# Optimization experiments

Measured on AMD Instinct MI355X. Metric: run time of the kernel, lower is better.

The kernel has to match this reference:

```python
import jax, jax.numpy as jnp
import numpy as np

EPS = 1e-5
GROUPS = 4


def _bn(x, g, b, axes):
    # training-mode batch norm (fresh torch module runs in train mode): biased var
    mean = x.mean(axes, keepdims=True)
    var = x.var(axes, keepdims=True)
    sh = (1, -1) + (1,) * (x.ndim - 2)
    return (x - mean) * jax.lax.rsqrt(var + EPS) * g.reshape(sh) + b.reshape(sh)


def _prelu(x, a):
    return jnp.where(x >= 0, x, a * x)


def _avgpool2(x):
    B, C, H, W = x.shape
    return x.reshape(B, C, H // 2, 2, W // 2, 2).mean(axis=(3, 5))


def _axial(x, dim, qkv_w, qkv_g, qkv_b, sim_g, sim_b, rel_emb, out_g, out_b):
    # x: [B, C, H, W]; dim==0 attends over H, dim==1 over W
    if dim == 0:
        x = jnp.transpose(x, (0, 3, 1, 2))  # [B, W, C, H]
    else:
        x = jnp.transpose(x, (0, 2, 1, 3))  # [B, H, C, W]
    B, D1, C, A = x.shape
    x = x.reshape(B * D1, C, A)
    # 1x1 conv1d (no bias) + BN1d
    qkv = jnp.einsum('oc,nca->noa', qkv_w, x)
    qkv = _bn(qkv, qkv_g, qkv_b, axes=(0, 2))
    gc = qkv.shape[1] // GROUPS // 2  # group_channels
    qkv = qkv.reshape(B * D1, GROUPS, 2 * gc, A)
    q = qkv[:, :, : gc // 2]
    k = qkv[:, :, gc // 2: gc]
    v = qkv[:, :, gc:]
    # relative position embeddings gathered into [2*gc, A, A]
    ri = jnp.arange(A)[:, None] - jnp.arange(A)[None, :] + A - 1  # [A, A]
    emb = rel_emb[:, ri]
    qe, ke, ve = emb[: gc // 2], emb[gc // 2: gc], emb[gc:]
    q_emb = jnp.einsum('ngci,cij->ngij', q, qe)
    k_emb = jnp.einsum('ngci,cij->ngij', k, ke)
    qk = jnp.einsum('ngci,ngcj->ngij', q_emb, k_emb)
    sim = jnp.concatenate([qk, q_emb, k_emb], axis=1)  # [N, 3g, A, A]
    sim = _bn(sim, sim_g, sim_b, axes=(0, 2, 3))
    sim = sim.reshape(B * D1, 3, GROUPS, A, A).sum(axis=1)
    sim = jax.nn.softmax(sim, axis=3)
    am = jnp.einsum('ngij,ngcj->ngci', sim, v)
    ame = jnp.einsum('ngij,cij->ngci', sim, ve)
    # cat along last dim then view -> equivalent to stacking pairs on a new axis
    out = jnp.stack([am, ame], axis=3).reshape(B * D1, 2 * GROUPS * gc, A)
    out = _bn(out, out_g, out_b, axes=(0, 2))
    out = out.reshape(B, D1, GROUPS * gc, 2, A).sum(axis=3)
    if dim == 0:
        return jnp.transpose(out, (0, 2, 3, 1))  # [B, C_out, H, W]
    return jnp.transpose(out, (0, 2, 1, 3))


def _cbn(x, g, b, lin_w, latent):
    x = _bn(x, g, b, axes=(0, 2, 3))
    sb = lin_w @ latent  # [2*C]
    C = x.shape[1]
    scale, bias = sb[:C], sb[C:]
    return scale[None, :, None, None] * x + bias[None, :, None, None]


def _forward(input, latent_vector, w_in, cbn1_g, cbn1_b, cbn1_lin, prelu1,
             ax0_qkv_w, ax0_qkv_g, ax0_qkv_b, ax0_sim_g, ax0_sim_b, ax0_rel_emb, ax0_out_g, ax0_out_b,
             ax1_qkv_w, ax1_qkv_g, ax1_qkv_b, ax1_sim_g, ax1_sim_b, ax1_rel_emb, ax1_out_g, ax1_out_b,
             w_out, cbn2_g, cbn2_b, cbn2_lin, prelu2):
    out = jnp.einsum('oc,bchw->bohw', w_in, input)
    out = _prelu(_cbn(out, cbn1_g, cbn1_b, cbn1_lin, latent_vector), prelu1)
    out = _axial(out, 0, ax0_qkv_w, ax0_qkv_g, ax0_qkv_b, ax0_sim_g, ax0_sim_b, ax0_rel_emb, ax0_out_g, ax0_out_b)
    out = _axial(out, 1, ax1_qkv_w, ax1_qkv_g, ax1_qkv_b, ax1_sim_g, ax1_sim_b, ax1_rel_emb, ax1_out_g, ax1_out_b)
    out = _avgpool2(out)
    out = jnp.einsum('oc,bchw->bohw', w_out, out)
    out = _cbn(out, cbn2_g, cbn2_b, cbn2_lin, latent_vector)
    out = out + _avgpool2(input)  # residual_mapping is Identity (in==out channels)
    return _prelu(out, prelu2)


def setup_inputs() -> dict:
    key = jax.random.key(0)
    ks = jax.random.split(key, 12)
    C, L, S = 64, 256, 128
    gc = C // GROUPS  # 16
    d = {}
    d['input'] = jax.random.normal(ks[0], (4, C, S, S), dtype=jnp.float32)
    d['latent_vector'] = jax.random.normal(ks[1], (L,), dtype=jnp.float32)
    d['w_in'] = jax.random.normal(ks[2], (C, C), dtype=jnp.float32) * 0.1
    d['cbn1_g'] = jnp.ones((C,), jnp.float32)
    d['cbn1_b'] = jnp.zeros((C,), jnp.float32)
    d['cbn1_lin'] = jax.random.normal(ks[3], (2 * C, L), dtype=jnp.float32) * 0.05
    d['prelu1'] = jnp.float32(0.25)
    for i, k1, k2 in [(0, ks[4], ks[5]), (1, ks[6], ks[7])]:
        d[f'ax{i}_qkv_w'] = jax.random.normal(k1, (2 * C, C), dtype=jnp.float32) * 0.1
        d[f'ax{i}_qkv_g'] = jnp.ones((2 * C,), jnp.float32)
        d[f'ax{i}_qkv_b'] = jnp.zeros((2 * C,), jnp.float32)
        d[f'ax{i}_sim_g'] = jnp.ones((3 * GROUPS,), jnp.float32)
        d[f'ax{i}_sim_b'] = jnp.zeros((3 * GROUPS,), jnp.float32)
        d[f'ax{i}_rel_emb'] = jax.random.normal(k2, (2 * gc, 2 * S - 1), dtype=jnp.float32)
        d[f'ax{i}_out_g'] = jnp.ones((2 * C,), jnp.float32)
        d[f'ax{i}_out_b'] = jnp.zeros((2 * C,), jnp.float32)
    d['w_out'] = jax.random.normal(ks[8], (C, C), dtype=jnp.float32) * 0.1
    d['cbn2_g'] = jnp.ones((C,), jnp.float32)
    d['cbn2_b'] = jnp.zeros((C,), jnp.float32)
    d['cbn2_lin'] = jax.random.normal(ks[9], (2 * C, L), dtype=jnp.float32) * 0.05
    d['prelu2'] = jnp.float32(0.25)
    return d


def reference(input, latent_vector, w_in, cbn1_g, cbn1_b, cbn1_lin, prelu1,
              ax0_qkv_w, ax0_qkv_g, ax0_qkv_b, ax0_sim_g, ax0_sim_b, ax0_rel_emb, ax0_out_g, ax0_out_b,
              ax1_qkv_w, ax1_qkv_g, ax1_qkv_b, ax1_sim_g, ax1_sim_b, ax1_rel_emb, ax1_out_g, ax1_out_b,
              w_out, cbn2_g, cbn2_b, cbn2_lin, prelu2):
    return _forward(input, latent_vector, w_in, cbn1_g, cbn1_b, cbn1_lin, prelu1,
                    ax0_qkv_w, ax0_qkv_g, ax0_qkv_b, ax0_sim_g, ax0_sim_b, ax0_rel_emb, ax0_out_g, ax0_out_b,
                    ax1_qkv_w, ax1_qkv_g, ax1_qkv_b, ax1_sim_g, ax1_sim_b, ax1_rel_emb, ax1_out_g, ax1_out_b,
                    w_out, cbn2_g, cbn2_b, cbn2_lin, prelu2)
```

## Files before the change

kernel.cpp:

```cpp
#include <hip/hip_runtime.h>

#define EPS 1e-5f
#define SP 16

typedef __attribute__((ext_vector_type(4))) _Float16 h4;
typedef __attribute__((ext_vector_type(8))) _Float16 h8;
typedef __attribute__((ext_vector_type(4))) float f4;
typedef __attribute__((ext_vector_type(4))) unsigned int u4;

#define WS_SB1        0
#define WS_SB2        128
#define WS_STAT_C1    256
#define WS_STAT_QKV0  2304
#define WS_STAT_QKV1  6400
#define WS_STAT_SIM0  10496
#define WS_STAT_SIM1  10880
#define WS_STAT_OUT0  11264
#define WS_STAT_OUT1  15360
#define WS_STAT_C2    19456
#define WS_STAT_END   21504

#define WS_R1  32768
#define WS_R2  (WS_R1 + 8388608)
#define WS_R3  (WS_R2 + 8388608)

#define SIM_CNT_INV (1.f / 2097152.f)

#define L_QEA 0
#define L_KEB 32768
#define L_RET 65536
#define L_AQ  73728
#define L_AK  77824
#define L_V   73728

__device__ __forceinline__ float wred(float v) {
    #pragma unroll
    for (int off = 32; off > 0; off >>= 1) v += __shfl_down(v, off, 64);
    return v;
}

__global__ void k_prep0(const float* __restrict__ lin1, const float* __restrict__ lin2,
                        const float* __restrict__ latent, float* __restrict__ ws) {
    int t = threadIdx.x;
    for (int i = 256 + t; i < WS_STAT_END; i += 256) ws[i] = 0.f;
    const float* lin = (t < 128) ? lin1 : lin2;
    int row = t & 127;
    float s = 0.f;
    for (int l = 0; l < 256; ++l) s += lin[row * 256 + l] * latent[l];
    ws[(t < 128 ? WS_SB1 : WS_SB2) + row] = s;
}

__global__ __launch_bounds__(256) void k_conv1(const float* __restrict__ in,
                                               const float* __restrict__ w,
                                               float* __restrict__ out) {
    __shared__ float ws_[4096];
    int t = threadIdx.x;
    for (int i = t; i < 4096; i += 256) ws_[i] = w[i];
    __syncthreads();
    int p  = blockIdx.x * 256 + t;
    int b  = p >> 14, hw = p & 16383;
    const float* ip = in + b * 64 * 16384 + hw;
    float x[64];
    #pragma unroll
    for (int c = 0; c < 64; ++c) x[c] = ip[c * 16384];
    float* op = out + b * 64 * 16384 + hw;
    for (int o = 0; o < 64; ++o) {
        float acc = 0.f;
        #pragma unroll
        for (int c = 0; c < 64; ++c) acc += ws_[o * 64 + c] * x[c];
        op[o * 16384] = acc;
    }
}

__global__ void k_stats(const float* __restrict__ src, int C, int logK, int MK, int split,
                        float* __restrict__ stat) {
    int c = blockIdx.x % C;
    int chunk = blockIdx.x / C;
    int per = MK / split;
    int base = chunk * per;
    int Km1 = (1 << logK) - 1;
    float s = 0.f, ss = 0.f;
    for (int i = base + threadIdx.x; i < base + per; i += blockDim.x) {
        int m = i >> logK, k = i & Km1;
        float v = src[((m * C + c) << logK) + k];
        s += v; ss += v * v;
    }
    s = wred(s); ss = wred(ss);
    if ((threadIdx.x & 63) == 0) { atomicAdd(&stat[c * SP], s); atomicAdd(&stat[(C + c) * SP], ss); }
}

__global__ __launch_bounds__(256) void k_t1t(const float* __restrict__ src, float* __restrict__ dst,
                                             const float* __restrict__ ws,
                                             const float* __restrict__ g1,
                                             const float* __restrict__ b1,
                                             const float* __restrict__ prelu1) {
    __shared__ float tile[32][33];
    int bid = blockIdx.x;
    int wt = bid & 3, ht = (bid >> 2) & 3, c = (bid >> 4) & 63, b = bid >> 10;
    float mean = ws[WS_STAT_C1 + c * SP] * (1.f / 65536.f);
    float var  = ws[WS_STAT_C1 + (64 + c) * SP] * (1.f / 65536.f) - mean * mean;
    float ab = g1[c] * rsqrtf(var + EPS);
    float sc = ws[WS_SB1 + c], bi = ws[WS_SB1 + 64 + c];
    float A = sc * ab;
    float Bb = sc * (b1[c] - mean * ab) + bi;
    float slope = *prelu1;
    int tx = threadIdx.x & 31, ty = threadIdx.x >> 5;
    const float* sp = src + ((b * 64 + c) * 128 + ht * 32) * 128 + wt * 32;
    for (int r = 0; r < 4; ++r) {
        float v = sp[(ty + r * 8) * 128 + tx];
        v = A * v + Bb;
        v = v >= 0.f ? v : slope * v;
        tile[ty + r * 8][tx] = v;
    }
    __syncthreads();
    float* dp = dst + b * 1048576 + (wt * 32) * 8192 + c * 128 + ht * 32;
    for (int r = 0; r < 4; ++r)
        dp[(ty + r * 8) * 8192 + tx] = tile[tx][ty + r * 8];
}

__global__ __launch_bounds__(256) void k_qkvm(const float* __restrict__ x, const float* __restrict__ w,
                                              _Float16* __restrict__ out, float* __restrict__ statq,
                                              int SB, int SR, int SC) {
    __shared__ __align__(16) _Float16 Wh[8192];
    __shared__ __align__(16) _Float16 Xt[8192];
    int t = threadIdx.x;
    int lane = t & 63, wv = t >> 6;
    int l15 = lane & 15, g4 = lane >> 4;
    int n = (blockIdx.x & 7) * 64 + (blockIdx.x >> 3);
    int b = n >> 7, r = n & 127;
    for (int i = t; i < 8192; i += 256) {
        int o = i >> 6, c = i & 63;
        Wh[o * 64 + (c ^ ((o & 7) << 3))] = (_Float16)w[i];
    }
    const float* xp = x + b * SB + r * SR;
    for (int i = t; i < 8192; i += 256) {
        int c = i >> 7, a = i & 127;
        Xt[a * 64 + (c ^ ((a & 7) << 3))] = (_Float16)xp[c * SC + a];
    }
    __syncthreads();
    _Float16* op = out + n * 16384;
    float sA[2][4] = {{0.f,0.f,0.f,0.f},{0.f,0.f,0.f,0.f}};
    float qA[2][4] = {{0.f,0.f,0.f,0.f},{0.f,0.f,0.f,0.f}};
    #pragma unroll
    for (int ot2 = 0; ot2 < 2; ++ot2) {
        int orow = (wv * 2 + ot2) * 16 + l15;
        h8 af[2];
        #pragma unroll
        for (int kk = 0; kk < 2; ++kk)
            af[kk] = *(const h8*)&Wh[orow * 64 + ((kk * 32 + g4 * 8) ^ ((orow & 7) << 3))];
        #pragma unroll
        for (int at = 0; at < 8; ++at) {
            int arow = at * 16 + l15;
            f4 c4 = {0.f, 0.f, 0.f, 0.f};
            #pragma unroll
            for (int kk = 0; kk < 2; ++kk) {
                h8 bf = *(const h8*)&Xt[arow * 64 + ((kk * 32 + g4 * 8) ^ ((arow & 7) << 3))];
                c4 = __builtin_amdgcn_mfma_f32_16x16x32_f16(af[kk], bf, c4, 0, 0, 0);
            }
            #pragma unroll
            for (int r4 = 0; r4 < 4; ++r4) {
                int o = (wv * 2 + ot2) * 16 + g4 * 4 + r4;
                float v = c4[r4];
                op[o * 128 + at * 16 + l15] = (_Float16)v;
                sA[ot2][r4] += v; qA[ot2][r4] += v * v;
            }
        }
    }
    #pragma unroll
    for (int ot2 = 0; ot2 < 2; ++ot2)
        #pragma unroll
        for (int r4 = 0; r4 < 4; ++r4) {
            float s = sA[ot2][r4], ss = qA[ot2][r4];
            #pragma unroll
            for (int msk = 1; msk < 16; msk <<= 1) {
                s += __shfl_xor(s, msk, 64); ss += __shfl_xor(ss, msk, 64);
            }
            if (l15 == 0) {
                int o = (wv * 2 + ot2) * 16 + g4 * 4 + r4;
                atomicAdd(&statq[o * SP], s);
                atomicAdd(&statq[(128 + o) * SP], ss);
            }
        }
}

__device__ __forceinline__ void stage_aqk(unsigned char* L, const _Float16* qkv,
                                          const float* statq, const float* qg, const float* qb,
                                          int n, int g, int t) {
    const _Float16* qp = qkv + n * 16384 + g * 32 * 128;
    #pragma unroll
    for (int k = 0; k < 4; ++k) {
        int i = t + k * 512;
        int a = i & 127, cc = i >> 7;
        int ch = g * 32 + cc;
        float mean = statq[ch * SP] * (1.f / 65536.f);
        float var  = statq[(128 + ch) * SP] * (1.f / 65536.f) - mean * mean;
        float A = qg[ch] * rsqrtf(var + EPS);
        float B = qb[ch] - mean * A;
        float v = A * (float)qp[cc * 128 + a] + B;
        _Float16 h = (_Float16)v;
        int off = a * 32 + ((cc * 2) ^ ((a & 4) << 2));
        *(_Float16*)(L + L_AQ + off) = (cc < 8) ? h : (_Float16)0.f;
        *(_Float16*)(L + L_AK + off) = (cc < 8) ? (_Float16)0.f : h;
    }
}

__device__ __forceinline__ void stage_ret(unsigned char* L, const float* remb, int crow0, int t) {
    #pragma unroll
    for (int k = 0; k < 8; ++k) {
        int i = t + k * 512;
        int d = i & 255, c = i >> 8;
        float v = (d < 255) ? remb[(crow0 + c) * 255 + d] : 0.f;
        *(_Float16*)(L + L_RET + d * 32 + ((c * 2) ^ ((d & 4) << 2))) = (_Float16)v;
    }
}

template <bool STATS>
__device__ __forceinline__ void build_emb(unsigned char* L, int w, int l15, int g4, float* s) {
    int at = w;
    int arow = at * 16 + l15;
    int aoff = arow * 32 + ((g4 * 8) ^ ((arow & 4) << 2));
    h4 aq = *(const h4*)(L + L_AQ + aoff);
    h4 ak = *(const h4*)(L + L_AK + aoff);
    int abase = at * 16 + g4 * 4;
    #pragma unroll
    for (int m = 0; m < 9; ++m) {
        int drow = (at + m) * 16 + l15;
        h4 bf = *(const h4*)(L + L_RET + drow * 32 + ((g4 * 8) ^ ((drow & 4) << 2)));
        f4 z = {0.f, 0.f, 0.f, 0.f};
        f4 dq = __builtin_amdgcn_mfma_f32_16x16x16f16(aq, bf, z, 0, 0, 0);
        f4 dk = __builtin_amdgcn_mfma_f32_16x16x16f16(ak, bf, z, 0, 0, 0);
        #pragma unroll
        for (int r = 0; r < 4; ++r) {
            int a = abase + r;
            int b = 127 + a - drow;
            bool ok = (m == 0 || m == 8) ? (b >= 0 && b < 128) : true;
            if (ok) {
                int off = b * 256 + ((a * 2) ^ ((b & 7) << 4));
                *(_Float16*)(L + L_QEA + off) = (_Float16)dq[r];
                *(_Float16*)(L + L_KEB + off) = (_Float16)dk[r];
                if (STATS) {
                    s[0] += dq[r]; s[1] += dq[r] * dq[r];
                    s[2] += dk[r]; s[3] += dk[r] * dk[r];
                }
            }
        }
    }
}

__device__ __forceinline__ void qk_mfma(unsigned char* L, int i0, int l15, int g4, f4 acc[8]) {
    h8 af[4];
    #pragma unroll
    for (int ks = 0; ks < 4; ++ks) {
        int row = i0 + l15;
        af[ks] = *(const h8*)(L + L_QEA + row * 256 + ((ks * 64 + g4 * 16) ^ ((row & 7) << 4)));
    }
    #pragma unroll
    for (int tj = 0; tj < 8; ++tj) {
        h8 bf[4];
        #pragma unroll
        for (int ks = 0; ks < 4; ++ks) {
            int row = tj * 16 + l15;
            bf[ks] = *(const h8*)(L + L_KEB + row * 256 + ((ks * 64 + g4 * 16) ^ ((row & 7) << 4)));
        }
        f4 c = {0.f, 0.f, 0.f, 0.f};
        #pragma unroll
        for (int ks = 0; ks < 4; ++ks)
            c = __builtin_amdgcn_mfma_f32_16x16x32_f16(af[ks], bf[ks], c, 0, 0, 0);
        acc[tj] = c;
    }
}

__global__ __launch_bounds__(512, 4) void k_passA(const _Float16* __restrict__ qkv,
                                                  const float* __restrict__ remb,
                                                  const float* __restrict__ statq,
                                                  const float* __restrict__ qg,
                                                  const float* __restrict__ qb,
                                                  float* __restrict__ statsim) {
    __shared__ __align__(16) unsigned char L[81920];
    int t = threadIdx.x;
    int lane = t & 63, w = t >> 6;
    int l15 = lane & 15, g4 = lane >> 4;
    int ts = (blockIdx.x & 7) * 64 + (blockIdx.x >> 3);
    int n = (ts >> 2) * 4, g = ts & 3;

    stage_aqk(L, qkv, statq, qg, qb, n, g, t);
    stage_ret(L, remb, 0, t);
    __syncthreads();

    float es[4] = {0.f, 0.f, 0.f, 0.f};
    build_emb<true>(L, w, l15, g4, es);
    __syncthreads();

    float* red = (float*)(L + L_AK);
    #pragma unroll
    for (int k = 0; k < 4; ++k) es[k] = wred(es[k]);
    if (lane == 0) {
        red[w * 4 + 0] = es[0]; red[w * 4 + 1] = es[1];
        red[w * 4 + 2] = es[2]; red[w * 4 + 3] = es[3];
    }

    f4 acc[8];
    qk_mfma(L, w * 16, l15, g4, acc);

    float s = 0.f, ss = 0.f;
    #pragma unroll
    for (int tj = 0; tj < 8; ++tj)
        #pragma unroll
        for (int r = 0; r < 4; ++r) { float x = acc[tj][r]; s += x; ss += x * x; }
    s = wred(s); ss = wred(ss);
    if (lane == 0) { red[32 + w * 2] = s; red[33 + w * 2] = ss; }
    __syncthreads();

    if (t < 6) {
        float v = 0.f;
        int dst;
        if (t == 0)      { for (int k = 0; k < 8; ++k) v += red[32 + 2 * k]; dst = g; }
        else if (t == 1) { for (int k = 0; k < 8; ++k) v += red[33 + 2 * k]; dst = 12 + g; }
        else if (t == 2) { for (int k = 0; k < 8; ++k) v += red[k * 4 + 0];  dst = 4 + g; }
        else if (t == 3) { for (int k = 0; k < 8; ++k) v += red[k * 4 + 1];  dst = 16 + g; }
        else if (t == 4) { for (int k = 0; k < 8; ++k) v += red[k * 4 + 2];  dst = 8 + g; }
        else             { for (int k = 0; k < 8; ++k) v += red[k * 4 + 3];  dst = 20 + g; }
        atomicAdd(&statsim[dst * SP], v);
    }
}

__global__ __launch_bounds__(512, 4) void k_passB(const _Float16* __restrict__ qkv,
                                                  const float* __restrict__ remb,
                                                  const float* __restrict__ statq,
                                                  const float* __restrict__ qg,
                                                  const float* __restrict__ qb,
                                                  const float* __restrict__ statsim,
                                                  const float* __restrict__ simg,
                                                  const float* __restrict__ simb,
                                                  unsigned int* __restrict__ att2,
                                                  float* __restrict__ statout) {
    __shared__ __align__(16) unsigned char L[81920];
    int t = threadIdx.x;
    int lane = t & 63, w = t >> 6;
    int l15 = lane & 15, g4 = lane >> 4;
    int s0 = (blockIdx.x & 7) * 256 + (blockIdx.x >> 3);
    int n = s0 >> 2, g = s0 & 3;

    stage_aqk(L, qkv, statq, qg, qb, n, g, t);
    stage_ret(L, remb, 0, t);
    __syncthreads();

    build_emb<false>(L, w, l15, g4, nullptr);
    __syncthreads();

    #pragma unroll
    for (int k = 0; k < 4; ++k) {
        int i = t + k * 512;
        int j = i & 127, c = i >> 7;
        int ch = g * 32 + 16 + c;
        float mean = statq[ch * SP] * (1.f / 65536.f);
        float var  = statq[(128 + ch) * SP] * (1.f / 65536.f) - mean * mean;
        float A = qg[ch] * rsqrtf(var + EPS);
        float B = qb[ch] - mean * A;
        float v = A * (float)qkv[n * 16384 + ch * 128 + j] + B;
        *(_Float16*)(L + L_V + c * 256 + ((j * 2) ^ ((c & 7) << 4))) = (_Float16)v;
    }
    #pragma unroll
    for (int k = 0; k < 8; ++k) {
        int i = t + k * 512;
        int d = i & 255, c = i >> 8;
        float v = (d < 255) ? remb[(16 + c) * 255 + d] : 0.f;
        *(_Float16*)(L + L_RET + c * 512 + ((d * 2) ^ ((c & 7) << 4))) = (_Float16)v;
    }

    int i0 = w * 16;
    f4 acc[8];
    qk_mfma(L, i0, l15, g4, acc);

    float Aqk, Aqe, Ake, Cst = 0.f;
    {
        float A3[3];
        #pragma unroll
        for (int k = 0; k < 3; ++k) {
            int ch = k * 4 + g;
            float mean = statsim[ch * SP] * SIM_CNT_INV;
            float var  = statsim[(12 + ch) * SP] * SIM_CNT_INV - mean * mean;
            float A = simg[ch] * rsqrtf(var + EPS);
            A3[k] = A;
            Cst += simb[ch] - mean * A;
        }
        Aqk = A3[0]; Aqe = A3[1]; Ake = A3[2];
    }
    int ib = (i0 + g4 * 4) * 2;
    #pragma unroll
    for (int tj = 0; tj < 8; ++tj) {
        int j = tj * 16 + l15;
        h4 q4 = *(const h4*)(L + L_QEA + j * 256 + (ib ^ ((j & 7) << 4)));
        h4 k4 = *(const h4*)(L + L_KEB + j * 256 + (ib ^ ((j & 7) << 4)));
        #pragma unroll
        for (int r = 0; r < 4; ++r)
            acc[tj][r] = Aqk * acc[tj][r] + Aqe * (float)q4[r] + Ake * (float)k4[r] + Cst;
    }

    float inv4[4];
    #pragma unroll
    for (int r = 0; r < 4; ++r) {
        float m = acc[0][r];
        #pragma unroll
        for (int tj = 1; tj < 8; ++tj) m = fmaxf(m, acc[tj][r]);
        #pragma unroll
        for (int msk = 1; msk < 16; msk <<= 1) m = fmaxf(m, __shfl_xor(m, msk, 64));
        float s = 0.f;
        #pragma unroll
        for (int tj = 0; tj < 8; ++tj) {
            float e = __expf(acc[tj][r] - m);
            acc[tj][r] = e; s += e;
        }
        #pragma unroll
        for (int msk = 1; msk < 16; msk <<= 1) s += __shfl_xor(s, msk, 64);
        inv4[r] = 1.f / s;
    }

    _Float16 ph[4][8];
    #pragma unroll
    for (int r = 0; r < 4; ++r)
        #pragma unroll
        for (int tj = 0; tj < 8; ++tj)
            ph[r][tj] = (_Float16)(acc[tj][r] * inv4[r]);
    __syncthreads();

    #pragma unroll
    for (int r = 0; r < 4; ++r) {
        int i = i0 + g4 * 4 + r;
        int swz = (i & 7) << 4;
        #pragma unroll
        for (int tj = 0; tj < 8; ++tj) {
            int j = tj * 16 + l15;
            _Float16 h = ph[r][tj];
            *(_Float16*)(L + L_QEA + i * 256 + ((j * 2) ^ swz)) = h;
            int cl = (j >= i) ? (127 + i - j) : j;
            *(_Float16*)(L + L_KEB + i * 256 + ((cl * 2) ^ swz)) = (j >= i) ? h : (_Float16)0.f;
        }
    }
    __syncthreads();

    h8 vf[4], vef[4];
    #pragma unroll
    for (int ks = 0; ks < 4; ++ks) {
        vf[ks]  = *(const h8*)(L + L_V   + l15 * 256 + ((ks * 64 + g4 * 16) ^ ((l15 & 7) << 4)));
        vef[ks] = *(const h8*)(L + L_RET + l15 * 512 + ((ks * 64 + g4 * 16) ^ ((l15 & 7) << 4)));
    }
    int row = i0 + l15;
    int sw = (row & 7) << 4;
    f4 cam = {0.f, 0.f, 0.f, 0.f}, cae = {0.f, 0.f, 0.f, 0.f};
    #pragma unroll
    for (int ks = 0; ks < 4; ++ks) {
        h8 pf  = *(const h8*)(L + L_QEA + row * 256 + ((ks * 64 + g4 * 16) ^ sw));
        h8 plf = *(const h8*)(L + L_KEB + row * 256 + ((ks * 64 + g4 * 16) ^ sw));
        cam = __builtin_amdgcn_mfma_f32_16x16x32_f16(vf[ks],  pf,  cam, 0, 0, 0);
        cae = __builtin_amdgcn_mfma_f32_16x16x32_f16(vef[ks], plf, cae, 0, 0, 0);
    }
    __syncthreads();

    #pragma unroll
    for (int r = 0; r < 4; ++r) {
        int i = i0 + g4 * 4 + r;
        int swz = (i & 7) << 4;
        #pragma unroll
        for (int tj = 0; tj < 8; ++tj) {
            int j = tj * 16 + l15;
            int cl = (j < i) ? (i - 1 - j) : j;
            *(_Float16*)(L + L_KEB + i * 256 + ((cl * 2) ^ swz)) = (j < i) ? ph[r][tj] : (_Float16)0.f;
        }
    }
    __syncthreads();

    h8 vef2[4];
    #pragma unroll
    for (int ks = 0; ks < 4; ++ks)
        vef2[ks] = *(const h8*)(L + L_RET + l15 * 512 + ((256 + ks * 64 + g4 * 16) ^ ((l15 & 7) << 4)));
    #pragma unroll
    for (int ks = 0; ks < 4; ++ks) {
        h8 phf = *(const h8*)(L + L_KEB + row * 256 + ((ks * 64 + g4 * 16) ^ sw));
        cae = __builtin_amdgcn_mfma_f32_16x16x32_f16(vef2[ks], phf, cae, 0, 0, 0);
    }

    unsigned int* attL = (unsigned int*)(L + L_QEA);
    int i = i0 + l15;
    #pragma unroll
    for (int r = 0; r < 4; ++r) {
        union { _Float16 h[2]; unsigned int u; } pk;
        pk.h[0] = (_Float16)cam[r];
        pk.h[1] = (_Float16)cae[r];
        attL[(g4 * 4 + r) * 128 + i] = pk.u;
    }

    float* sred = (float*)(L + L_KEB);
    #pragma unroll
    for (int r = 0; r < 4; ++r) {
        float sa = cam[r], qa = cam[r] * cam[r];
        float se = cae[r], qe = cae[r] * cae[r];
        #pragma unroll
        for (int msk = 1; msk < 16; msk <<= 1) {
            sa += __shfl_xor(sa, msk, 64); qa += __shfl_xor(qa, msk, 64);
            se += __shfl_xor(se, msk, 64); qe += __shfl_xor(qe, msk, 64);
        }
        if (l15 == 0) {
            int base = w * 64 + g4 * 16 + r * 4;
            sred[base + 0] = sa; sred[base + 1] = qa;
            sred[base + 2] = se; sred[base + 3] = qe;
        }
    }
    __syncthreads();

    unsigned int* ab = att2 + n * 8192 + g * 2048;
    *(u4*)(ab + t * 4) = *(const u4*)(attL + t * 4);

    if (t < 64) {
        int lc = t & 31, stat = t >> 5;
        int c = lc >> 1, s = lc & 1;
        int gg4 = c >> 2, r = c & 3;
        float v = 0.f;
        #pragma unroll
        for (int ww = 0; ww < 8; ++ww)
            v += sred[ww * 64 + gg4 * 16 + r * 4 + 2 * s + stat];
        atomicAdd(&statout[(stat * 128 + g * 32 + lc) * SP], v);
    }
}

__global__ __launch_bounds__(256) void k_finish0(const unsigned int* __restrict__ att2,
                                                 const float* __restrict__ statout,
                                                 const float* __restrict__ og,
                                                 const float* __restrict__ ob,
                                                 float* __restrict__ t2) {
    __shared__ float tile[8][32][33];
    __shared__ float cf[256];
    int t = threadIdx.x;
    if (t < 128) {
        float mean = statout[t * SP] * (1.f / 65536.f);
        float var  = statout[(128 + t) * SP] * (1.f / 65536.f) - mean * mean;
        float A = og[t] * rsqrtf(var + EPS);
        cf[t] = A;
        cf[128 + t] = ob[t] - mean * A;
    }
    __syncthreads();
    int bid = blockIdx.x;
    int wt = bid & 3, ht = (bid >> 2) & 3, cg = (bid >> 4) & 7, b = bid >> 7;
    for (int i = t; i < 8192; i += 256) {
        int h = i & 31, w = (i >> 5) & 31, cl = i >> 10;
        int c_out = cg * 8 + cl;
        int chg = (c_out >> 4) * 32 + (c_out & 15) * 2;
        int p = chg >> 1;
        union { unsigned int u; _Float16 h2[2]; } pk;
        pk.u = att2[((b * 128 + wt * 32 + w) * 64 + p) * 128 + ht * 32 + h];
        tile[cl][w][h] = cf[chg] * (float)pk.h2[0] + cf[128 + chg]
                       + cf[chg + 1] * (float)pk.h2[1] + cf[129 + chg];
    }
    __syncthreads();
    for (int i = t; i < 8192; i += 256) {
        int w = i & 31, h = (i >> 5) & 31, cl = i >> 10;
        t2[((b * 64 + cg * 8 + cl) * 128 + ht * 32 + h) * 128 + wt * 32 + w] = tile[cl][w][h];
    }
}

__global__ __launch_bounds__(64) void k_conv2f(const unsigned int* __restrict__ att2,
                                               const float* __restrict__ statout,
                                               const float* __restrict__ og,
                                               const float* __restrict__ ob,
                                               const float* __restrict__ w,
                                               float* __restrict__ out,
                                               float* __restrict__ statc2) {
    __shared__ float ws_[4096];
    __shared__ float cf[4][64];
    __shared__ float otile[64][65];
    int t = threadIdx.x;
    for (int i = t; i < 4096; i += 64) ws_[i] = w[i];
    {
        int chg = (t >> 4) * 32 + (t & 15) * 2;
        float m0 = statout[chg * SP] * (1.f / 65536.f);
        float v0 = statout[(128 + chg) * SP] * (1.f / 65536.f) - m0 * m0;
        float A0 = og[chg] * rsqrtf(v0 + EPS);
        cf[0][t] = A0; cf[1][t] = ob[chg] - m0 * A0;
        float m1 = statout[(chg + 1) * SP] * (1.f / 65536.f);
        float v1 = statout[(129 + chg) * SP] * (1.f / 65536.f) - m1 * m1;
        float A1 = og[chg + 1] * rsqrtf(v1 + EPS);
        cf[2][t] = A1; cf[3][t] = ob[chg + 1] - m1 * A1;
    }
    __syncthreads();
    int p = blockIdx.x * 64 + t;
    int b = p >> 12, yx = p & 4095, y = yx >> 6, x = yx & 63;
    const unsigned int* ap = att2 + (b * 128 + 2 * y) * 8192 + 2 * x;
    float xc[64];
    #pragma unroll
    for (int c = 0; c < 64; ++c) {
        int pp = (c >> 4) * 16 + (c & 15);
        const unsigned int* q = ap + pp * 128;
        union { unsigned int u; _Float16 h2[2]; } a0, a1, a2, a3;
        a0.u = q[0]; a1.u = q[1]; a2.u = q[8192]; a3.u = q[8193];
        float s0 = (float)a0.h2[0] + (float)a1.h2[0] + (float)a2.h2[0] + (float)a3.h2[0];
        float s1 = (float)a0.h2[1] + (float)a1.h2[1] + (float)a2.h2[1] + (float)a3.h2[1];
        xc[c] = 0.25f * (cf[0][c] * s0 + cf[2][c] * s1) + cf[1][c] + cf[3][c];
    }
    float* op = out + b * 262144 + yx;
    for (int o = 0; o < 64; ++o) {
        float acc = 0.f;
        #pragma unroll
        for (int c = 0; c < 64; ++c) acc += ws_[o * 64 + c] * xc[c];
        op[o * 4096] = acc;
        otile[o][t] = acc;
    }
    __syncthreads();
    float s = 0.f, ss = 0.f;
    #pragma unroll
    for (int k = 0; k < 64; ++k) { float v = otile[t][k]; s += v; ss += v * v; }
    atomicAdd(&statc2[t * SP], s);
    atomicAdd(&statc2[(64 + t) * SP], ss);
}

__global__ __launch_bounds__(256) void k_final(const float* __restrict__ c2out,
                                               const float* __restrict__ input,
                                               const float* __restrict__ ws,
                                               const float* __restrict__ g2,
                                               const float* __restrict__ b2,
                                               const float* __restrict__ prelu2,
                                               float* __restrict__ out) {
    int q = blockIdx.x * 256 + threadIdx.x;
    int x4 = (q & 15) << 2, y = (q >> 4) & 63, o = (q >> 10) & 63, b = q >> 16;
    float mean = ws[WS_STAT_C2 + o * SP] * (1.f / 16384.f);
    float var  = ws[WS_STAT_C2 + (64 + o) * SP] * (1.f / 16384.f) - mean * mean;
    float ab = g2[o] * rsqrtf(var + EPS);
    float sc = ws[WS_SB2 + o], bi = ws[WS_SB2 + 64 + o];
    float A = sc * ab;
    float B = sc * (b2[o] - mean * ab) + bi;
    float slope = *prelu2;
    int base = ((b * 64 + o) * 64 + y) * 64 + x4;
    float4 c = *(const float4*)&c2out[base];
    const float* ip = input + ((b * 64 + o) * 128 + 2 * y) * 128 + 2 * x4;
    float4 r0a = *(const float4*)&ip[0];
    float4 r0b = *(const float4*)&ip[4];
    float4 r1a = *(const float4*)&ip[128];
    float4 r1b = *(const float4*)&ip[132];
    float4 r;
    float v0 = A * c.x + B + 0.25f * (r0a.x + r0a.y + r1a.x + r1a.y);
    float v1 = A * c.y + B + 0.25f * (r0a.z + r0a.w + r1a.z + r1a.w);
    float v2 = A * c.z + B + 0.25f * (r0b.x + r0b.y + r1b.x + r1b.y);
    float v3 = A * c.w + B + 0.25f * (r0b.z + r0b.w + r1b.z + r1b.w);
    r.x = v0 >= 0.f ? v0 : slope * v0;
    r.y = v1 >= 0.f ? v1 : slope * v1;
    r.z = v2 >= 0.f ? v2 : slope * v2;
    r.w = v3 >= 0.f ? v3 : slope * v3;
    *(float4*)&out[base] = r;
}

extern "C" void kernel_launch(void* const* d_in, const int* in_sizes, int n_in,
                              void* d_out, int out_size, void* d_ws, size_t ws_size,
                              hipStream_t stream) {
    const float* input    = (const float*)d_in[0];
    const float* latent   = (const float*)d_in[1];
    const float* w_in     = (const float*)d_in[2];
    const float* cbn1_g   = (const float*)d_in[3];
    const float* cbn1_b   = (const float*)d_in[4];
    const float* cbn1_lin = (const float*)d_in[5];
    const float* prelu1   = (const float*)d_in[6];
    const float* ax_qkv_w[2] = {(const float*)d_in[7],  (const float*)d_in[15]};
    const float* ax_qkv_g[2] = {(const float*)d_in[8],  (const float*)d_in[16]};
    const float* ax_qkv_b[2] = {(const float*)d_in[9],  (const float*)d_in[17]};
    const float* ax_sim_g[2] = {(const float*)d_in[10], (const float*)d_in[18]};
    const float* ax_sim_b[2] = {(const float*)d_in[11], (const float*)d_in[19]};
    const float* ax_rel[2]   = {(const float*)d_in[12], (const float*)d_in[20]};
    const float* ax_out_g[2] = {(const float*)d_in[13], (const float*)d_in[21]};
    const float* ax_out_b[2] = {(const float*)d_in[14], (const float*)d_in[22]};
    const float* w_out    = (const float*)d_in[23];
    const float* cbn2_g   = (const float*)d_in[24];
    const float* cbn2_b   = (const float*)d_in[25];
    const float* cbn2_lin = (const float*)d_in[26];
    const float* prelu2   = (const float*)d_in[27];

    float* ws    = (float*)d_ws;
    float* out0  = ws + WS_R1;
    float* t1t   = ws + WS_R1 + 4194304;
    unsigned int* att2 = (unsigned int*)(ws + WS_R1);
    _Float16* qkvh = (_Float16*)(ws + WS_R2);
    float* t23   = ws + WS_R3;
    float* c2o   = ws + WS_R3;
    float* dst   = (float*)d_out;

    k_prep0<<<1, 256, 0, stream>>>(cbn1_lin, cbn2_lin, latent, ws);
    k_conv1<<<256, 256, 0, stream>>>(input, w_in, out0);
    k_stats<<<1024, 256, 0, stream>>>(out0, 64, 14, 65536, 16, ws + WS_STAT_C1);
    k_t1t<<<4096, 256, 0, stream>>>(out0, t1t, ws, cbn1_g, cbn1_b, prelu1);

    k_qkvm<<<512, 256, 0, stream>>>(t1t, ax_qkv_w[0], qkvh, ws + WS_STAT_QKV0,
                                    1048576, 8192, 128);
    k_passA<<<512, 512, 0, stream>>>(qkvh, ax_rel[0], ws + WS_STAT_QKV0,
                                     ax_qkv_g[0], ax_qkv_b[0], ws + WS_STAT_SIM0);
    k_passB<<<2048, 512, 0, stream>>>(qkvh, ax_rel[0], ws + WS_STAT_QKV0,
                                      ax_qkv_g[0], ax_qkv_b[0], ws + WS_STAT_SIM0,
                                      ax_sim_g[0], ax_sim_b[0], att2, ws + WS_STAT_OUT0);
    k_finish0<<<512, 256, 0, stream>>>(att2, ws + WS_STAT_OUT0, ax_out_g[0], ax_out_b[0], t23);

    k_qkvm<<<512, 256, 0, stream>>>(t23, ax_qkv_w[1], qkvh, ws + WS_STAT_QKV1,
                                    1048576, 128, 16384);
    k_passA<<<512, 512, 0, stream>>>(qkvh, ax_rel[1], ws + WS_STAT_QKV1,
                                     ax_qkv_g[1], ax_qkv_b[1], ws + WS_STAT_SIM1);
    k_passB<<<2048, 512, 0, stream>>>(qkvh, ax_rel[1], ws + WS_STAT_QKV1,
                                      ax_qkv_g[1], ax_qkv_b[1], ws + WS_STAT_SIM1,
                                      ax_sim_g[1], ax_sim_b[1], att2, ws + WS_STAT_OUT1);

    k_conv2f<<<256, 64, 0, stream>>>(att2, ws + WS_STAT_OUT1, ax_out_g[1], ax_out_b[1],
                                     w_out, c2o, ws + WS_STAT_C2);
    k_final<<<1024, 256, 0, stream>>>(c2o, input, ws, cbn2_g, cbn2_b, prelu2, dst);
}
```

Baseline: 350.6 us.

## Fuse conv1 BN stats into conv, split output channels, merge ve-attention MFMA passes

Conv1 now computes per-channel sum and sum-of-squares with wave reductions and atomics, which removes the separate k_stats pass over the conv output. Its grid is doubled by splitting the output channels in half per block, which raises parallelism but reads the input twice. In passB the relative-embedding attention now writes the full diagonal-shifted probability band into one wider LDS buffer. This replaces two half-passes with zero masking and an extra sync with a single 8-step MFMA loop, at the cost of zero-filling LDS and reusing regions with new layout offsets.

```diff
diff --git a/kernel.cpp b/kernel.cpp
--- a/kernel.cpp
+++ b/kernel.cpp
@@ -52,41 +52,37 @@
 
 __global__ __launch_bounds__(256) void k_conv1(const float* __restrict__ in,
                                                const float* __restrict__ w,
-                                               float* __restrict__ out) {
-    __shared__ float ws_[4096];
+                                               float* __restrict__ out,
+                                               float* __restrict__ stat) {
+    __shared__ float ws_[2048];
+    __shared__ float sred[2][4][32];
     int t = threadIdx.x;
-    for (int i = t; i < 4096; i += 256) ws_[i] = w[i];
-    __syncthreads();
-    int p  = blockIdx.x * 256 + t;
+    int lane = t & 63, wv = t >> 6;
+    int oh = blockIdx.x & 1;
+    int pb = blockIdx.x >> 1;
+    for (int i = t; i < 2048; i += 256) ws_[i] = w[oh * 2048 + i];
+    __syncthreads();
+    int p  = pb * 256 + t;
     int b  = p >> 14, hw = p & 16383;
     const float* ip = in + b * 64 * 16384 + hw;
     float x[64];
     #pragma unroll
     for (int c = 0; c < 64; ++c) x[c] = ip[c * 16384];
-    float* op = out + b * 64 * 16384 + hw;
-    for (int o = 0; o < 64; ++o) {
+    float* op = out + b * 64 * 16384 + hw + oh * 32 * 16384;
+    for (int o2 = 0; o2 < 32; ++o2) {
         float acc = 0.f;
         #pragma unroll
-        for (int c = 0; c < 64; ++c) acc += ws_[o * 64 + c] * x[c];
-        op[o * 16384] = acc;
-    }
-}
-
-__global__ void k_stats(const float* __restrict__ src, int C, int logK, int MK, int split,
-                        float* __restrict__ stat) {
-    int c = blockIdx.x % C;
-    int chunk = blockIdx.x / C;
-    int per = MK / split;
-    int base = chunk * per;
-    int Km1 = (1 << logK) - 1;
-    float s = 0.f, ss = 0.f;
-    for (int i = base + threadIdx.x; i < base + per; i += blockDim.x) {
-        int m = i >> logK, k = i & Km1;
-        float v = src[((m * C + c) << logK) + k];
-        s += v; ss += v * v;
-    }
-    s = wred(s); ss = wred(ss);
-    if ((threadIdx.x & 63) == 0) { atomicAdd(&stat[c * SP], s); atomicAdd(&stat[(C + c) * SP], ss); }
+        for (int c = 0; c < 64; ++c) acc += ws_[o2 * 64 + c] * x[c];
+        op[o2 * 16384] = acc;
+        float s = wred(acc), ss = wred(acc * acc);
+        if (lane == 0) { sred[0][wv][o2] = s; sred[1][wv][o2] = ss; }
+    }
+    __syncthreads();
+    if (t < 64) {
+        int o2 = t & 31, st = t >> 5;
+        float v = sred[st][0][o2] + sred[st][1][o2] + sred[st][2][o2] + sred[st][3][o2];
+        atomicAdd(&stat[(st * 64 + oh * 32 + o2) * SP], v);
+    }
 }
 
 __global__ __launch_bounds__(256) void k_t1t(const float* __restrict__ src, float* __restrict__ dst,
@@ -431,56 +427,75 @@
         #pragma unroll
         for (int tj = 0; tj < 8; ++tj) {
             int j = tj * 16 + l15;
-            _Float16 h = ph[r][tj];
-            *(_Float16*)(L + L_QEA + i * 256 + ((j * 2) ^ swz)) = h;
-            int cl = (j >= i) ? (127 + i - j) : j;
-            *(_Float16*)(L + L_KEB + i * 256 + ((cl * 2) ^ swz)) = (j >= i) ? h : (_Float16)0.f;
-        }
-    }
-    __syncthreads();
-
-    h8 vf[4], vef[4];
-    #pragma unroll
-    for (int ks = 0; ks < 4; ++ks) {
-        vf[ks]  = *(const h8*)(L + L_V   + l15 * 256 + ((ks * 64 + g4 * 16) ^ ((l15 & 7) << 4)));
-        vef[ks] = *(const h8*)(L + L_RET + l15 * 512 + ((ks * 64 + g4 * 16) ^ ((l15 & 7) << 4)));
-    }
+            *(_Float16*)(L + L_QEA + i * 256 + ((j * 2) ^ swz)) = ph[r][tj];
+        }
+    }
+    if (w >= 4) {
+        #pragma unroll
+        for (int z = 0; z < 8; ++z) {
+            u4 zz = {0u, 0u, 0u, 0u};
+            *(u4*)(L + w * 8192 + (z * 64 + lane) * 16) = zz;
+        }
+        #pragma unroll
+        for (int r = 0; r < 4; ++r) {
+            int i = i0 + g4 * 4 + r;
+            int swz = (i & 7) << 4;
+            #pragma unroll
+            for (int tj = 0; tj < 8; ++tj) {
+                int j = tj * 16 + l15;
+                int d = 127 + i - j;
+                *(_Float16*)(L + i * 512 + ((d * 2) ^ swz)) = ph[r][tj];
+            }
+        }
+    }
+    __syncthreads();
+
+    h8 vf[4];
+    #pragma unroll
+    for (int ks = 0; ks < 4; ++ks)
+        vf[ks] = *(const h8*)(L + L_V + l15 * 256 + ((ks * 64 + g4 * 16) ^ ((l15 & 7) << 4)));
     int row = i0 + l15;
     int sw = (row & 7) << 4;
-    f4 cam = {0.f, 0.f, 0.f, 0.f}, cae = {0.f, 0.f, 0.f, 0.f};
+    f4 cam = {0.f, 0.f, 0.f, 0.f};
     #pragma unroll
     for (int ks = 0; ks < 4; ++ks) {
-        h8 pf  = *(const h8*)(L + L_QEA + row * 256 + ((ks * 64 + g4 * 16) ^ sw));
-        h8 plf = *(const h8*)(L + L_KEB + row * 256 + ((ks * 64 + g4 * 16) ^ sw));
-        cam = __builtin_amdgcn_mfma_f32_16x16x32_f16(vf[ks],  pf,  cam, 0, 0, 0);
-        cae = __builtin_amdgcn_mfma_f32_16x16x32_f16(vef[ks], plf, cae, 0, 0, 0);
-    }
-    __syncthreads();
-
-    #pragma unroll
-    for (int r = 0; r < 4; ++r) {
-        int i = i0 + g4 * 4 + r;
-        int swz = (i & 7) << 4;
-        #pragma unroll
-        for (int tj = 0; tj < 8; ++tj) {
-            int j = tj * 16 + l15;
-            int cl = (j < i) ? (i - 1 - j) : j;
-            *(_Float16*)(L + L_KEB + i * 256 + ((cl * 2) ^ swz)) = (j < i) ? ph[r][tj] : (_Float16)0.f;
-        }
-    }
-    __syncthreads();
-
-    h8 vef2[4];
-    #pragma unroll
-    for (int ks = 0; ks < 4; ++ks)
-        vef2[ks] = *(const h8*)(L + L_RET + l15 * 512 + ((256 + ks * 64 + g4 * 16) ^ ((l15 & 7) << 4)));
-    #pragma unroll
-    for (int ks = 0; ks < 4; ++ks) {
-        h8 phf = *(const h8*)(L + L_KEB + row * 256 + ((ks * 64 + g4 * 16) ^ sw));
-        cae = __builtin_amdgcn_mfma_f32_16x16x32_f16(vef2[ks], phf, cae, 0, 0, 0);
-    }
-
-    unsigned int* attL = (unsigned int*)(L + L_QEA);
+        h8 pf = *(const h8*)(L + L_QEA + row * 256 + ((ks * 64 + g4 * 16) ^ sw));
+        cam = __builtin_amdgcn_mfma_f32_16x16x32_f16(vf[ks], pf, cam, 0, 0, 0);
+    }
+    __syncthreads();
+
+    if (w < 4) {
+        #pragma unroll
+        for (int z = 0; z < 8; ++z) {
+            u4 zz = {0u, 0u, 0u, 0u};
+            *(u4*)(L + w * 8192 + (z * 64 + lane) * 16) = zz;
+        }
+        #pragma unroll
+        for (int r = 0; r < 4; ++r) {
+            int i = i0 + g4 * 4 + r;
+            int swz = (i & 7) << 4;
+            #pragma unroll
+            for (int tj = 0; tj < 8; ++tj) {
+                int j = tj * 16 + l15;
+                int d = 127 + i - j;
+                *(_Float16*)(L + i * 512 + ((d * 2) ^ swz)) = ph[r][tj];
+            }
+        }
+    }
+    __syncthreads();
+
+    h8 vef[8];
+    #pragma unroll
+    for (int ks = 0; ks < 8; ++ks)
+        vef[ks] = *(const h8*)(L + L_RET + l15 * 512 + ((ks * 64 + g4 * 16) ^ ((l15 & 7) << 4)));
+    f4 cae = {0.f, 0.f, 0.f, 0.f};
+    #pragma unroll
+    for (int ks = 0; ks < 8; ++ks) {
+        h8 phf = *(const h8*)(L + row * 512 + ((ks * 64 + g4 * 16) ^ sw));
+        cae = __builtin_amdgcn_mfma_f32_16x16x32_f16(vef[ks], phf, cae, 0, 0, 0);
+    }
+
+    unsigned int* attL = (unsigned int*)(L + L_V);
     int i = i0 + l15;
     #pragma unroll
     for (int r = 0; r < 4; ++r) {
@@ -490,7 +505,7 @@
         attL[(g4 * 4 + r) * 128 + i] = pk.u;
     }
 
-    float* sred = (float*)(L + L_KEB);
+    float* sredW = (float*)(L + w * 8192);
     #pragma unroll
     for (int r = 0; r < 4; ++r) {
         float sa = cam[r], qa = cam[r] * cam[r];
@@ -501,9 +516,9 @@
             se += __shfl_xor(se, msk, 64); qe += __shfl_xor(qe, msk, 64);
         }
         if (l15 == 0) {
-            int base = w * 64 + g4 * 16 + r * 4;
-            sred[base + 0] = sa; sred[base + 1] = qa;
-            sred[base + 2] = se; sred[base + 3] = qe;
+            int base = g4 * 16 + r * 4;
+            sredW[base + 0] = sa; sredW[base + 1] = qa;
+            sredW[base + 2] = se; sredW[base + 3] = qe;
         }
     }
     __syncthreads();
@@ -518,7 +533,7 @@
         float v = 0.f;
         #pragma unroll
         for (int ww = 0; ww < 8; ++ww)
-            v += sred[ww * 64 + gg4 * 16 + r * 4 + 2 * s + stat];
+            v += ((const float*)L)[ww * 2048 + gg4 * 16 + r * 4 + 2 * s + stat];
         atomicAdd(&statout[(stat * 128 + g * 32 + lc) * SP], v);
     }
 }
@@ -681,8 +696,7 @@
     float* dst   = (float*)d_out;
 
     k_prep0<<<1, 256, 0, stream>>>(cbn1_lin, cbn2_lin, latent, ws);
-    k_conv1<<<256, 256, 0, stream>>>(input, w_in, out0);
-    k_stats<<<1024, 256, 0, stream>>>(out0, 64, 14, 65536, 16, ws + WS_STAT_C1);
+    k_conv1<<<512, 256, 0, stream>>>(input, w_in, out0, ws + WS_STAT_C1);
     k_t1t<<<4096, 256, 0, stream>>>(out0, t1t, ws, cbn1_g, cbn1_b, prelu1);
 
     k_qkvm<<<512, 256, 0, stream>>>(t1t, ax_qkv_w[0], qkvh, ws + WS_STAT_QKV0,
```

Result: faster. 335.6 us (-4.3%).
